# Kernel tuning notes

Hardware: AMD Instinct MI355X
Metric: run time of the kernel (lower is better)

The kernel has to match this reference:

```python
import jax, jax.numpy as jnp
import numpy as np

B, T, F, H = 8192, 256, 64, 50

def setup_inputs() -> dict:
    key = jax.random.key(0)
    ks = jax.random.split(key, 6)
    s = 0.1
    x = jax.random.normal(ks[0], (B, T, F), dtype=jnp.float32)
    W = jax.random.normal(ks[1], (F, 3 * H), dtype=jnp.float32) * s   # input kernel [z|r|h]
    U = jax.random.normal(ks[2], (H, 3 * H), dtype=jnp.float32) * s   # recurrent kernel
    b = jax.random.normal(ks[3], (2, 3 * H), dtype=jnp.float32) * s   # [input bias; recurrent bias] (reset_after=True)
    Wd = jax.random.normal(ks[4], (H, 1), dtype=jnp.float32) * s
    bd = jax.random.normal(ks[5], (1,), dtype=jnp.float32) * s
    return {"x": x, "W": W, "U": U, "b": b, "Wd": Wd, "bd": bd}

def _gru_last_hidden(x, W, U, b):
    # Precompute input projections for all timesteps: [B,T,3H]
    xp = jnp.einsum('btf,fg->btg', x, W) + b[0]
    xp = jnp.transpose(xp, (1, 0, 2))  # [T,B,3H] for scan over time
    bi = b[1]

    def step(h, xt):
        rp = h @ U + bi                       # recurrent projection [B,3H]
        xz, xr, xh = jnp.split(xt, 3, axis=-1)
        rz, rr, rh = jnp.split(rp, 3, axis=-1)
        z = jax.nn.sigmoid(xz + rz)
        r = jax.nn.sigmoid(xr + rr)
        hh = jnp.tanh(xh + r * rh)            # reset_after=True formulation
        h_new = z * h + (1.0 - z) * hh
        return h_new, None

    h0 = jnp.zeros((x.shape[0], U.shape[0]), dtype=x.dtype)
    h_last, _ = jax.lax.scan(step, h0, xp)
    return h_last

def reference(x, W, U, b, Wd, bd):
    h = _gru_last_hidden(x, W, U, b)   # [B,H]
    # Dropout is identity at inference time
    return h @ Wd + bd                 # [B,1]
```

## Files before the change

### kernel.cpp

```cpp
#include <hip/hip_runtime.h>
#include <hip/hip_bf16.h>


typedef __attribute__((ext_vector_type(8))) short s16x8;
typedef __attribute__((ext_vector_type(4))) short s16x4;
typedef __attribute__((ext_vector_type(4))) float f32x4;

#define TS 256

__device__ __forceinline__ unsigned short f2bf(float f) {
  return __builtin_bit_cast(unsigned short, __float2bfloat16(f));
}

#define RAWBAR()                                                \
  do {                                                          \
    asm volatile("s_waitcnt lgkmcnt(0)" ::: "memory");          \
    __builtin_amdgcn_sched_barrier(0);                          \
    __builtin_amdgcn_s_barrier();                               \
  } while (0)

__global__ __launch_bounds__(256, 2) void gru_fused(
    const float* __restrict__ x,  const float* __restrict__ W,
    const float* __restrict__ U,  const float* __restrict__ b,
    const float* __restrict__ Wd, const float* __restrict__ bdp,
    float* __restrict__ out)
{
  __shared__ __align__(16) unsigned short xbuf[2][2][512];
  __shared__ __align__(16) unsigned short hbuf[2][2][512];
  __shared__ float red[4][16];

  const int tid = threadIdx.x;
  const int l   = tid & 63;
  const int w   = tid >> 6;
  const int lhi = l >> 4, llo = l & 15;
  const int row0 = blockIdx.x << 4;
  const int u = (w << 4) + llo;

  ((unsigned long long*)hbuf)[tid]       = 0ULL;
  ((unsigned long long*)hbuf)[tid + 256] = 0ULL;

  float bz = 0.f, br = 0.f, bh0 = 0.f, bh1 = 0.f;
  if (u < 50) {
    bz  = b[u]       + b[150 + u];
    br  = b[50 + u]  + b[200 + u];
    bh0 = b[100 + u];
    bh1 = b[250 + u];
  }

  s16x8 breg[3][4];
  #pragma unroll
  for (int g = 0; g < 3; ++g) {
    #pragma unroll
    for (int kc = 0; kc < 4; ++kc) {
      s16x8 f;
      #pragma unroll
      for (int i = 0; i < 8; ++i) {
        const int k = kc * 32 + lhi * 8 + i;
        float v = 0.f;
        if (u < 50 && k < 114)
          v = (k < 64) ? W[k * 150 + g * 50 + u]
                       : U[(k - 64) * 150 + g * 50 + u];
        f[i] = (short)f2bf(v);
      }
      breg[g][kc] = f;
    }
  }

  const int sc    = tid >> 7;
  const int sla   = (tid >> 1) & 63;
  const int shalf = tid & 1;
  const float* xp = x + (long)(row0 + (sla & 15)) * (TS * 64)
                      + sc * 32 + (sla >> 4) * 8 + shalf * 4;
  unsigned short* const xdst0 = &xbuf[0][sc][sla * 8 + shalf * 4];
  unsigned short* const xdst1 = &xbuf[1][sc][sla * 8 + shalf * 4];

  {
    const f32x4 x0 = *(const f32x4*)xp;
    s16x4 pk;
    pk[0] = (short)f2bf(x0[0]); pk[1] = (short)f2bf(x0[1]);
    pk[2] = (short)f2bf(x0[2]); pk[3] = (short)f2bf(x0[3]);
    *(s16x4*)xdst0 = pk;
  }
  f32x4 xA0 = *(const f32x4*)(xp + 1 * 64);
  f32x4 xA1 = *(const f32x4*)(xp + 2 * 64);
  f32x4 xA2 = *(const f32x4*)(xp + 3 * 64);
  f32x4 xA3 = *(const f32x4*)(xp + 4 * 64);
  f32x4 xB0, xB1, xB2, xB3;
  RAWBAR();

  float h0 = 0.f, h1 = 0.f, h2 = 0.f, h3 = 0.f;

#define GRU_STEP(T, CUR, NXT, PR, XDST)                                        \
  {                                                                            \
    const int tl = ((T) + 5 > TS - 1) ? (TS - 1) : ((T) + 5);                  \
    NXT = *(const f32x4*)(xp + (long)tl * 64);                                 \
    const s16x8 a0 = *(const s16x8*)&xbuf[PR][0][l * 8];                       \
    const s16x8 a1 = *(const s16x8*)&xbuf[PR][1][l * 8];                       \
    const s16x8 a2 = *(const s16x8*)&hbuf[PR][0][l * 8];                       \
    const s16x8 a3 = *(const s16x8*)&hbuf[PR][1][l * 8];                       \
    f32x4 lo[3], hi[3];                                                        \
    _Pragma("unroll")                                                          \
    for (int g = 0; g < 3; ++g) {                                              \
      f32x4 zz = {0.f, 0.f, 0.f, 0.f};                                         \
      zz    = __builtin_amdgcn_mfma_f32_16x16x32_bf16(a2, breg[g][2], zz, 0,0,0);\
      hi[g] = __builtin_amdgcn_mfma_f32_16x16x32_bf16(a3, breg[g][3], zz, 0,0,0);\
      f32x4 yy = {0.f, 0.f, 0.f, 0.f};                                         \
      yy    = __builtin_amdgcn_mfma_f32_16x16x32_bf16(a0, breg[g][0], yy, 0,0,0);\
      lo[g] = __builtin_amdgcn_mfma_f32_16x16x32_bf16(a1, breg[g][1], yy, 0,0,0);\
    }                                                                          \
    {                                                                          \
      s16x4 pk;                                                                \
      pk[0] = (short)f2bf(CUR[0]); pk[1] = (short)f2bf(CUR[1]);                \
      pk[2] = (short)f2bf(CUR[2]); pk[3] = (short)f2bf(CUR[3]);                \
      *(s16x4*)(XDST) = pk;                                                    \
    }                                                                          \
    _Pragma("unroll")                                                          \
    for (int r = 0; r < 4; ++r) {                                              \
      float hv = (r == 0) ? h0 : (r == 1) ? h1 : (r == 2) ? h2 : h3;           \
      const float zs = lo[0][r] + hi[0][r] + bz;                               \
      const float rs = lo[1][r] + hi[1][r] + br;                               \
      const float z  = __builtin_amdgcn_rcpf(1.f + __expf(-zs));               \
      const float rr = __builtin_amdgcn_rcpf(1.f + __expf(-rs));               \
      const float ar = lo[2][r] + bh0 + rr * (hi[2][r] + bh1);                 \
      const float e  = __expf(2.f * ar);                                       \
      const float hh = 1.f - 2.f * __builtin_amdgcn_rcpf(1.f + e);             \
      hv = hh + z * (hv - hh);                                                 \
      if (r == 0) h0 = hv; else if (r == 1) h1 = hv;                           \
      else if (r == 2) h2 = hv; else h3 = hv;                                  \
      hbuf[(PR) ^ 1][u >> 5]                                                   \
          [(((u & 31) >> 3) * 16 + lhi * 4 + r) * 8 + (u & 7)] = f2bf(hv);     \
    }                                                                          \
    RAWBAR();                                                                  \
  }

  for (int t = 0; t < TS; t += 8) {
    GRU_STEP(t + 0, xA0, xB0, 0, xdst1)
    GRU_STEP(t + 1, xA1, xB1, 1, xdst0)
    GRU_STEP(t + 2, xA2, xB2, 0, xdst1)
    GRU_STEP(t + 3, xA3, xB3, 1, xdst0)
    GRU_STEP(t + 4, xB0, xA0, 0, xdst1)
    GRU_STEP(t + 5, xB1, xA1, 1, xdst0)
    GRU_STEP(t + 6, xB2, xA2, 0, xdst1)
    GRU_STEP(t + 7, xB3, xA3, 1, xdst0)
  }
#undef GRU_STEP

  const float Wdv = (u < 50) ? Wd[u] : 0.f;
  float p0 = h0 * Wdv, p1 = h1 * Wdv, p2 = h2 * Wdv, p3 = h3 * Wdv;
  #pragma unroll
  for (int m = 1; m < 16; m <<= 1) {
    p0 += __shfl_xor(p0, m);
    p1 += __shfl_xor(p1, m);
    p2 += __shfl_xor(p2, m);
    p3 += __shfl_xor(p3, m);
  }
  if (llo == 0) {
    red[w][lhi * 4 + 0] = p0;
    red[w][lhi * 4 + 1] = p1;
    red[w][lhi * 4 + 2] = p2;
    red[w][lhi * 4 + 3] = p3;
  }
  __syncthreads();
  if (tid < 16)
    out[row0 + tid] =
        red[0][tid] + red[1][tid] + red[2][tid] + red[3][tid] + bdp[0];
}

extern "C" void kernel_launch(void* const* d_in, const int* in_sizes, int n_in,
                              void* d_out, int out_size, void* d_ws, size_t ws_size,
                              hipStream_t stream) {
  const float* x   = (const float*)d_in[0];
  const float* W   = (const float*)d_in[1];
  const float* U   = (const float*)d_in[2];
  const float* b   = (const float*)d_in[3];
  const float* Wd  = (const float*)d_in[4];
  const float* bdp = (const float*)d_in[5];
  float* out = (float*)d_out;
  gru_fused<<<dim3(512), dim3(256), 0, stream>>>(x, W, U, b, Wd, bdp, out);
}
```

Measured before the change: 783.7 us.

## Ping-pong two row groups per block, overlapping MFMA and gate phases

Merges two 16-row groups into one 512-thread block and staggers them by half a step. While one group runs its MFMA projections, the other runs the gate nonlinearities, with a barrier between phases. The aim is to hide the serial latency of the MFMA-then-transcendental chain in each recurrent step. In exchange, each step now has two block-wide barriers, grid occupancy per CU changes, and the last gate stage needs an epilogue.

```diff
diff --git a/kernel.cpp b/kernel.cpp
--- a/kernel.cpp
+++ b/kernel.cpp
@@ -19,25 +19,27 @@
     __builtin_amdgcn_s_barrier();                               \
   } while (0)
 
-__global__ __launch_bounds__(256, 2) void gru_fused(
+__global__ __launch_bounds__(512, 1) void gru_fused(
     const float* __restrict__ x,  const float* __restrict__ W,
     const float* __restrict__ U,  const float* __restrict__ b,
     const float* __restrict__ Wd, const float* __restrict__ bdp,
     float* __restrict__ out)
 {
-  __shared__ __align__(16) unsigned short xbuf[2][2][512];
-  __shared__ __align__(16) unsigned short hbuf[2][2][512];
-  __shared__ float red[4][16];
+  __shared__ __align__(16) unsigned short xbuf[2][2][2][512];
+  __shared__ __align__(16) unsigned short hbuf[2][2][2][512];
+  __shared__ float red[2][4][16];
 
   const int tid = threadIdx.x;
   const int l   = tid & 63;
   const int w   = tid >> 6;
+  const int grp = w >> 2;
+  const int wg  = w & 3;
   const int lhi = l >> 4, llo = l & 15;
-  const int row0 = blockIdx.x << 4;
-  const int u = (w << 4) + llo;
+  const int row0 = (blockIdx.x << 5) + (grp << 4);
+  const int u = (wg << 4) + llo;
 
   ((unsigned long long*)hbuf)[tid]       = 0ULL;
-  ((unsigned long long*)hbuf)[tid + 256] = 0ULL;
+  ((unsigned long long*)hbuf)[tid + 512] = 0ULL;
 
   float bz = 0.f, br = 0.f, bh0 = 0.f, bh1 = 0.f;
   if (u < 50) {
@@ -66,39 +68,43 @@
     }
   }
 
-  const int sc    = tid >> 7;
-  const int sla   = (tid >> 1) & 63;
-  const int shalf = tid & 1;
+  const int gt    = tid & 255;
+  const int sc    = gt >> 7;
+  const int sla   = (gt >> 1) & 63;
+  const int shalf = gt & 1;
   const float* xp = x + (long)(row0 + (sla & 15)) * (TS * 64)
                       + sc * 32 + (sla >> 4) * 8 + shalf * 4;
-  unsigned short* const xdst0 = &xbuf[0][sc][sla * 8 + shalf * 4];
-  unsigned short* const xdst1 = &xbuf[1][sc][sla * 8 + shalf * 4];
+  unsigned short* const xd0 = &xbuf[grp][0][sc][sla * 8 + shalf * 4];
+  unsigned short* const xd1 = &xbuf[grp][1][sc][sla * 8 + shalf * 4];
+  const int lead = 5 - grp;
 
   {
     const f32x4 x0 = *(const f32x4*)xp;
     s16x4 pk;
     pk[0] = (short)f2bf(x0[0]); pk[1] = (short)f2bf(x0[1]);
     pk[2] = (short)f2bf(x0[2]); pk[3] = (short)f2bf(x0[3]);
-    *(s16x4*)xdst0 = pk;
-  }
-  f32x4 xA0 = *(const f32x4*)(xp + 1 * 64);
-  f32x4 xA1 = *(const f32x4*)(xp + 2 * 64);
-  f32x4 xA2 = *(const f32x4*)(xp + 3 * 64);
-  f32x4 xA3 = *(const f32x4*)(xp + 4 * 64);
-  f32x4 xB0, xB1, xB2, xB3;
-  RAWBAR();
+    *(s16x4*)xd0 = pk;
+  }
+  const float* xq = xp + (long)(1 - grp) * 64;
+  f32x4 R0 = *(const f32x4*)(xq);
+  f32x4 R1 = *(const f32x4*)(xq + 64);
+  f32x4 R2 = *(const f32x4*)(xq + 128);
+  f32x4 R3 = *(const f32x4*)(xq + 192);
+  f32x4 S0, S1, S2, S3;
+  __syncthreads();
 
   float h0 = 0.f, h1 = 0.f, h2 = 0.f, h3 = 0.f;
-
-#define GRU_STEP(T, CUR, NXT, PR, XDST)                                        \
+  f32x4 lo[3], hi[3];
+
+#define MFMA_STAGE(T, NXT)                                                     \
   {                                                                            \
-    const int tl = ((T) + 5 > TS - 1) ? (TS - 1) : ((T) + 5);                  \
+    int tl = (T) + lead; if (tl > TS - 1) tl = TS - 1;                         \
     NXT = *(const f32x4*)(xp + (long)tl * 64);                                 \
-    const s16x8 a0 = *(const s16x8*)&xbuf[PR][0][l * 8];                       \
-    const s16x8 a1 = *(const s16x8*)&xbuf[PR][1][l * 8];                       \
-    const s16x8 a2 = *(const s16x8*)&hbuf[PR][0][l * 8];                       \
-    const s16x8 a3 = *(const s16x8*)&hbuf[PR][1][l * 8];                       \
-    f32x4 lo[3], hi[3];                                                        \
+    const int PAR = (T) & 1;                                                   \
+    const s16x8 a2 = *(const s16x8*)&hbuf[grp][PAR][0][l * 8];                 \
+    const s16x8 a3 = *(const s16x8*)&hbuf[grp][PAR][1][l * 8];                 \
+    const s16x8 a0 = *(const s16x8*)&xbuf[grp][PAR][0][l * 8];                 \
+    const s16x8 a1 = *(const s16x8*)&xbuf[grp][PAR][1][l * 8];                 \
     _Pragma("unroll")                                                          \
     for (int g = 0; g < 3; ++g) {                                              \
       f32x4 zz = {0.f, 0.f, 0.f, 0.f};                                         \
@@ -108,11 +114,16 @@
       yy    = __builtin_amdgcn_mfma_f32_16x16x32_bf16(a0, breg[g][0], yy, 0,0,0);\
       lo[g] = __builtin_amdgcn_mfma_f32_16x16x32_bf16(a1, breg[g][1], yy, 0,0,0);\
     }                                                                          \
+  }
+
+#define GATE_STAGE(S, CUR)                                                     \
+  {                                                                            \
+    const int PW = ((S) + 1) & 1;                                              \
     {                                                                          \
       s16x4 pk;                                                                \
       pk[0] = (short)f2bf(CUR[0]); pk[1] = (short)f2bf(CUR[1]);                \
       pk[2] = (short)f2bf(CUR[2]); pk[3] = (short)f2bf(CUR[3]);                \
-      *(s16x4*)(XDST) = pk;                                                    \
+      *(s16x4*)(PW ? xd1 : xd0) = pk;                                          \
     }                                                                          \
     _Pragma("unroll")                                                          \
     for (int r = 0; r < 4; ++r) {                                              \
@@ -127,23 +138,51 @@
       hv = hh + z * (hv - hh);                                                 \
       if (r == 0) h0 = hv; else if (r == 1) h1 = hv;                           \
       else if (r == 2) h2 = hv; else h3 = hv;                                  \
-      hbuf[(PR) ^ 1][u >> 5]                                                   \
+      hbuf[grp][PW][u >> 5]                                                    \
           [(((u & 31) >> 3) * 16 + lhi * 4 + r) * 8 + (u & 7)] = f2bf(hv);     \
     }                                                                          \
+  }
+
+#define ITER(T, CUR, NXT, SKIPB)                                               \
+  {                                                                            \
+    if (grp == 0) { MFMA_STAGE(T, NXT) }                                       \
+    else if (!(SKIPB)) { GATE_STAGE((T) - 1, CUR) }                            \
     RAWBAR();                                                                  \
+    if (grp == 0) { GATE_STAGE(T, CUR) }                                       \
+    else { MFMA_STAGE(T, NXT) }                                                \
+    RAWBAR();                                                                  \
   }
 
   for (int t = 0; t < TS; t += 8) {
-    GRU_STEP(t + 0, xA0, xB0, 0, xdst1)
-    GRU_STEP(t + 1, xA1, xB1, 1, xdst0)
-    GRU_STEP(t + 2, xA2, xB2, 0, xdst1)
-    GRU_STEP(t + 3, xA3, xB3, 1, xdst0)
-    GRU_STEP(t + 4, xB0, xA0, 0, xdst1)
-    GRU_STEP(t + 5, xB1, xA1, 1, xdst0)
-    GRU_STEP(t + 6, xB2, xA2, 0, xdst1)
-    GRU_STEP(t + 7, xB3, xA3, 1, xdst0)
-  }
-#undef GRU_STEP
+    ITER(t + 0, R0, S0, t == 0)
+    ITER(t + 1, R1, S1, 0)
+    ITER(t + 2, R2, S2, 0)
+    ITER(t + 3, R3, S3, 0)
+    ITER(t + 4, S0, R0, 0)
+    ITER(t + 5, S1, R1, 0)
+    ITER(t + 6, S2, R2, 0)
+    ITER(t + 7, S3, R3, 0)
+  }
+#undef ITER
+#undef GATE_STAGE
+#undef MFMA_STAGE
+
+  if (grp) {
+    #pragma unroll
+    for (int r = 0; r < 4; ++r) {
+      float hv = (r == 0) ? h0 : (r == 1) ? h1 : (r == 2) ? h2 : h3;
+      const float zs = lo[0][r] + hi[0][r] + bz;
+      const float rs = lo[1][r] + hi[1][r] + br;
+      const float z  = __builtin_amdgcn_rcpf(1.f + __expf(-zs));
+      const float rr = __builtin_amdgcn_rcpf(1.f + __expf(-rs));
+      const float ar = lo[2][r] + bh0 + rr * (hi[2][r] + bh1);
+      const float e  = __expf(2.f * ar);
+      const float hh = 1.f - 2.f * __builtin_amdgcn_rcpf(1.f + e);
+      hv = hh + z * (hv - hh);
+      if (r == 0) h0 = hv; else if (r == 1) h1 = hv;
+      else if (r == 2) h2 = hv; else h3 = hv;
+    }
+  }
 
   const float Wdv = (u < 50) ? Wd[u] : 0.f;
   float p0 = h0 * Wdv, p1 = h1 * Wdv, p2 = h2 * Wdv, p3 = h3 * Wdv;
@@ -155,15 +194,17 @@
     p3 += __shfl_xor(p3, m);
   }
   if (llo == 0) {
-    red[w][lhi * 4 + 0] = p0;
-    red[w][lhi * 4 + 1] = p1;
-    red[w][lhi * 4 + 2] = p2;
-    red[w][lhi * 4 + 3] = p3;
+    red[grp][wg][lhi * 4 + 0] = p0;
+    red[grp][wg][lhi * 4 + 1] = p1;
+    red[grp][wg][lhi * 4 + 2] = p2;
+    red[grp][wg][lhi * 4 + 3] = p3;
   }
   __syncthreads();
-  if (tid < 16)
-    out[row0 + tid] =
-        red[0][tid] + red[1][tid] + red[2][tid] + red[3][tid] + bdp[0];
+  if (tid < 32) {
+    const int g = tid >> 4, r = tid & 15;
+    out[(blockIdx.x << 5) + tid] =
+        red[g][0][r] + red[g][1][r] + red[g][2][r] + red[g][3][r] + bdp[0];
+  }
 }
 
 extern "C" void kernel_launch(void* const* d_in, const int* in_sizes, int n_in,
@@ -176,5 +217,5 @@
   const float* Wd  = (const float*)d_in[4];
   const float* bdp = (const float*)d_in[5];
   float* out = (float*)d_out;
-  gru_fused<<<dim3(512), dim3(256), 0, stream>>>(x, W, U, b, Wd, bdp, out);
+  gru_fused<<<dim3(256), dim3(512), 0, stream>>>(x, W, U, b, Wd, bdp, out);
 }
```

Measured after the change: 815.4 us. +4.0%, slower.
